# Kernel optimization log

Hardware: AMD Instinct MI355X
Metric: run time of the kernel (lower is better)

The kernel has to match this reference:

```python
import jax, jax.numpy as jnp
import numpy as np

D_STATE = 512
D_MODEL = 512
BATCH = 8
SEQ = 4096
DT_MIN, DT_MAX = 1e-3, 0.1
LN_EPS = 1e-5


def setup_inputs() -> dict:
    key = jax.random.key(0)
    ks = jax.random.split(key, 4)
    x = jax.random.normal(ks[0], (BATCH, SEQ, D_MODEL), dtype=jnp.float32)
    volatility_scale = jax.random.uniform(ks[1], (BATCH, SEQ, 1), dtype=jnp.float32)
    # parameters (mirroring the torch module's __init__)
    log_lambda_real = jnp.linspace(np.log(DT_MIN), np.log(DT_MAX), D_STATE).astype(jnp.float32)
    log_b = jax.random.uniform(ks[2], (D_STATE, 1), dtype=jnp.float32, minval=-0.5, maxval=0.5)
    c = jax.random.normal(ks[3], (1, D_STATE), dtype=jnp.float32) / np.sqrt(D_STATE)
    log_d = jnp.zeros((1,), jnp.float32)
    ts = np.array([1.0 / 24.0, 1.0, 5.0, 21.0, 63.0], np.float32)
    extra = np.linspace(63.0, 189.0, D_STATE - len(ts), dtype=np.float32)
    log_step = jnp.log(jnp.asarray(np.concatenate([ts, extra])))
    volatility_gate = jnp.ones((D_MODEL,), jnp.float32)
    alpha = jnp.asarray(0.7, jnp.float32)
    ln_weight = jnp.ones((D_STATE,), jnp.float32)
    ln_bias = jnp.zeros((D_STATE,), jnp.float32)
    return dict(x=x, volatility_scale=volatility_scale,
                log_lambda_real=log_lambda_real, log_b=log_b, c=c, log_d=log_d,
                log_step=log_step, volatility_gate=volatility_gate, alpha=alpha,
                ln_weight=ln_weight, ln_bias=ln_bias)


def reference(x, volatility_scale, log_lambda_real, log_b, c, log_d,
              log_step, volatility_gate, alpha, ln_weight, ln_bias):
    lam = -jnp.exp(log_lambda_real)              # [N], negative real poles
    step = jnp.exp(log_step)                     # [N], per-state timescale
    b = jnp.exp(log_b)[:, 0]                     # [N]
    d = jnp.exp(log_d)                           # [1], skip gain
    # bilinear (Tustin) discretization, paired per state
    z = step * lam                               # [N]
    a_disc = (2.0 + z) / (2.0 - z)               # [N]
    b_disc = step * (1.0 + a_disc) * b / 2.0     # [N]
    gate = jax.nn.sigmoid(volatility_gate)       # [D]
    c_vec = c[0]                                 # [N]

    def layer_norm(h):
        mu = jnp.mean(h, axis=-1, keepdims=True)
        var = jnp.var(h, axis=-1, keepdims=True)
        return (h - mu) * jax.lax.rsqrt(var + LN_EPS) * ln_weight + ln_bias

    def scan_step(h, inp):
        x_t, v_t = inp                           # [B,D], [B,1]
        h = a_disc * h + b_disc * x_t            # diagonal SSM update, [B,N]
        h = layer_norm(h)
        h = h / (1.0 + gate * v_t)               # volatility gating
        y_t = jnp.sum(h * c_vec, axis=-1, keepdims=True) + d * x_t  # [B,D]
        return h, y_t

    h0 = jnp.zeros((x.shape[0], a_disc.shape[0]), x.dtype)
    xs = (jnp.swapaxes(x, 0, 1), jnp.swapaxes(volatility_scale, 0, 1))  # time-major
    _, ys = jax.lax.scan(scan_step, h0, xs)      # [S,B,D]
    y = jnp.swapaxes(ys, 0, 1)                   # [B,S,D]
    al = jax.nn.sigmoid(alpha)
    return al * x + (1.0 - al) * y
```

## Files before the change

kernel.cpp:

```cpp
#include <hip/hip_runtime.h>
#include <cstdint>
#include <cstddef>

#define BATCH 8
#define SEQ   4096
#define DS    512
#define JPL   8
#define BLK   8
#define NBLK  (SEQ / BLK)

typedef float v2f __attribute__((ext_vector_type(2)));
typedef float v4f __attribute__((ext_vector_type(4)));

static __device__ __forceinline__ v2f lo2(v4f x) { return __builtin_shufflevector(x, x, 0, 1); }
static __device__ __forceinline__ v2f hi2(v4f x) { return __builtin_shufflevector(x, x, 2, 3); }

template <int CTRL>
__device__ __forceinline__ float dpp_add(float v) {
  int t = __builtin_amdgcn_update_dpp(0, __builtin_bit_cast(int, v), CTRL, 0xF, 0xF, true);
  return v + __builtin_bit_cast(float, t);
}
__device__ __forceinline__ float wave_sum64(float v) {
  v = dpp_add<0x111>(v);
  v = dpp_add<0x112>(v);
  v = dpp_add<0x114>(v);
  v = dpp_add<0x118>(v);
  v = dpp_add<0x142>(v);
  v = dpp_add<0x143>(v);
  return v;
}
__device__ __forceinline__ float bcast63(float v) {
  return __builtin_bit_cast(float, __builtin_amdgcn_readlane(__builtin_bit_cast(int, v), 63));
}

__device__ __forceinline__ void ld16(const float* g, float* l) {
  __builtin_amdgcn_global_load_lds(
      (const __attribute__((address_space(1))) void*)g,
      (__attribute__((address_space(3))) void*)l, 16, 0, 0);
}

__global__ __launch_bounds__(192, 1) void ssm_scan(
    const float* __restrict__ x, const float* __restrict__ vol,
    const float* __restrict__ llr, const float* __restrict__ logb,
    const float* __restrict__ cvec, const float* __restrict__ lstp,
    const float* __restrict__ vgat, const float* __restrict__ lnw,
    const float* __restrict__ lnb, float* __restrict__ sp)
{
  __shared__ float X0[4096], X1[4096];
  __shared__ float R0[4096], R1[4096];
  __shared__ float SC0[512], SC1[512];

  const int b    = blockIdx.x;
  const int lane = threadIdx.x & 63;
  const int wid  = threadIdx.x >> 6;

  if (wid == 1) {
    const float* xg = x + (size_t)b * SEQ * DS + lane * JPL;
    float* spb = sp + (size_t)b * SEQ;

    auto dma_blk = [&](int blk, float* Xs) {
#pragma unroll
      for (int u = 0; u < BLK; ++u) {
        const float* row = xg + (size_t)(blk * BLK + u) * DS;
        ld16(row,     Xs + u * 512);
        ld16(row + 4, Xs + u * 512 + 256);
      }
    };
    auto red_copy = [&](const float* SCs, int blk) {
      float s[BLK];
#pragma unroll
      for (int u = 0; u < BLK; ++u) s[u] = wave_sum64(SCs[u * 64 + lane]);
      if (lane == 63) {
#pragma unroll
        for (int u = 0; u < BLK; ++u) spb[blk * BLK + u] = s[u];
      }
    };

    dma_blk(0, X0);
    __syncthreads();
#pragma unroll 1
    for (int i2 = 0; i2 < NBLK; i2 += 2) {
      dma_blk(i2 + 1, X1);
      if (i2 > 0) red_copy(SC1, i2 - 1);
      __syncthreads();
      if (i2 + 2 < NBLK) dma_blk(i2 + 2, X0);
      red_copy(SC0, i2);
      __syncthreads();
    }
    red_copy(SC1, NBLK - 1);
  } else if (wid == 2) {
    v2f gate[4];
#pragma unroll
    for (int j = 0; j < JPL; ++j)
      gate[j >> 1][j & 1] = 1.0f / (1.0f + expf(-vgat[lane * JPL + j]));
    const float* vg = vol + (size_t)b * SEQ;

    auto rg_blk = [&](v4f Va, v4f Vb, float* Rs) {
#pragma unroll
      for (int u = 0; u < BLK; ++u) {
        float vt = (u < 4) ? Va[u] : Vb[u - 4];
        v4f r0, r1;
#pragma unroll
        for (int k = 0; k < 4; ++k) {
          v2f den = gate[k] * vt + 1.0f;
          float q0 = __builtin_amdgcn_rcpf(den.x);
          float q1 = __builtin_amdgcn_rcpf(den.y);
          if (k < 2) { r0[2 * k] = q0; r0[2 * k + 1] = q1; }
          else       { r1[2 * (k - 2)] = q0; r1[2 * (k - 2) + 1] = q1; }
        }
        *(v4f*)(Rs + u * 512 + lane * 4)       = r0;
        *(v4f*)(Rs + u * 512 + 256 + lane * 4) = r1;
      }
    };

    v4f V0a = *(const v4f*)(vg + 0), V0b = *(const v4f*)(vg + 4);
    v4f V1a = *(const v4f*)(vg + 8), V1b = *(const v4f*)(vg + 12);
    rg_blk(V0a, V0b, R0);
    __syncthreads();
#pragma unroll 1
    for (int i2 = 0; i2 < NBLK; i2 += 2) {
      if (i2 + 2 < NBLK) {
        V0a = *(const v4f*)(vg + (i2 + 2) * BLK);
        V0b = *(const v4f*)(vg + (i2 + 2) * BLK + 4);
      }
      rg_blk(V1a, V1b, R1);
      __syncthreads();
      if (i2 + 3 < NBLK) {
        V1a = *(const v4f*)(vg + (i2 + 3) * BLK);
        V1b = *(const v4f*)(vg + (i2 + 3) * BLK + 4);
      }
      if (i2 + 2 < NBLK) rg_blk(V0a, V0b, R0);
      __syncthreads();
    }
  } else {
    v2f a[4], bd[4], w[4], bias[4], cc[4];
#pragma unroll
    for (int j = 0; j < JPL; ++j) {
      int n = lane * JPL + j;
      float lam = -expf(llr[n]);
      float st  = expf(lstp[n]);
      float z   = st * lam;
      float ad  = (2.0f + z) / (2.0f - z);
      a[j >> 1][j & 1]    = ad;
      bd[j >> 1][j & 1]   = st * (1.0f + ad) * expf(logb[n]) * 0.5f;
      w[j >> 1][j & 1]    = lnw[n];
      bias[j >> 1][j & 1] = lnb[n];
      cc[j >> 1][j & 1]   = cvec[n];
    }
    v2f h[4];
#pragma unroll
    for (int k = 0; k < 4; ++k) h[k] = (v2f){0.0f, 0.0f};

    auto proc_blk = [&](const float* Xs, const float* Rs, float* SCs) {
#pragma unroll
      for (int u = 0; u < BLK; ++u) {
        v4f xx0 = *(const v4f*)(Xs + u * 512 + lane * 4);
        v4f xx1 = *(const v4f*)(Xs + u * 512 + 256 + lane * 4);
        v4f rr0 = *(const v4f*)(Rs + u * 512 + lane * 4);
        v4f rr1 = *(const v4f*)(Rs + u * 512 + 256 + lane * 4);
        v2f xs[4] = {lo2(xx0), hi2(xx0), lo2(xx1), hi2(xx1)};
        v2f rs[4] = {lo2(rr0), hi2(rr0), lo2(rr1), hi2(rr1)};

        v2f hr[4];
#pragma unroll
        for (int k = 0; k < 4; ++k)
          hr[k] = __builtin_elementwise_fma(a[k], h[k], bd[k] * xs[k]);

        v2f ts = (hr[0] + hr[1]) + (hr[2] + hr[3]);
        float s1 = ts.x + ts.y;
        v2f qs = (hr[0] * hr[0] + hr[1] * hr[1]) + (hr[2] * hr[2] + hr[3] * hr[3]);
        float s2 = qs.x + qs.y;

        s1 = bcast63(wave_sum64(s1));
        s2 = bcast63(wave_sum64(s2));
        float mu  = s1 * (1.0f / DS);
        float m2  = s2 * (1.0f / DS);
        float var = __builtin_fmaf(-mu, mu, m2);
        float inv = __builtin_amdgcn_rsqf(var + 1e-5f);

#pragma unroll
        for (int k = 0; k < 4; ++k) {
          v2f niw = w[k] * inv;
          v2f hb  = bias[k] - niw * mu;
          v2f hln = __builtin_elementwise_fma(hr[k], niw, hb);
          h[k] = hln * rs[k];
        }

        v2f d = h[0] * cc[0];
        d = __builtin_elementwise_fma(h[1], cc[1], d);
        d = __builtin_elementwise_fma(h[2], cc[2], d);
        d = __builtin_elementwise_fma(h[3], cc[3], d);
        SCs[u * 64 + lane] = d.x + d.y;
      }
    };

    __syncthreads();
#pragma unroll 1
    for (int i2 = 0; i2 < NBLK; i2 += 2) {
      proc_blk(X0, R0, SC0);
      __syncthreads();
      proc_blk(X1, R1, SC1);
      __syncthreads();
    }
  }
}

__global__ __launch_bounds__(256) void out_scalar(
    const float* __restrict__ x, const float* __restrict__ sp,
    const float* __restrict__ alpha_p, const float* __restrict__ logd_p,
    float* __restrict__ out)
{
  const int lane = threadIdx.x & 63;
  const size_t bt = (size_t)blockIdx.x * 4 + (threadIdx.x >> 6);

  float al   = 1.0f / (1.0f + expf(-alpha_p[0]));
  float dd   = expf(logd_p[0]);
  float coef = __builtin_fmaf(1.0f - al, dd, al);
  float c1   = 1.0f - al;

  float s = sp[bt] * c1;
  const v4f* x4 = (const v4f*)x;
  v4f* o4 = (v4f*)out;
  size_t base = bt * 128;
#pragma unroll
  for (int j = 0; j < 2; ++j) {
    size_t i = base + lane + (size_t)j * 64;
    v4f xv = x4[i];
    o4[i] = xv * coef + s;
  }
}

extern "C" void kernel_launch(void* const* d_in, const int* in_sizes, int n_in,
                              void* d_out, int out_size, void* d_ws, size_t ws_size,
                              hipStream_t stream) {
  const float* x    = (const float*)d_in[0];
  const float* vol  = (const float*)d_in[1];
  const float* llr  = (const float*)d_in[2];
  const float* logb = (const float*)d_in[3];
  const float* cvec = (const float*)d_in[4];
  const float* logd = (const float*)d_in[5];
  const float* lstp = (const float*)d_in[6];
  const float* vgat = (const float*)d_in[7];
  const float* alph = (const float*)d_in[8];
  const float* lnw  = (const float*)d_in[9];
  const float* lnb  = (const float*)d_in[10];
  float* sp   = (float*)d_ws;
  float* outf = (float*)d_out;

  ssm_scan<<<BATCH, 192, 0, stream>>>(x, vol, llr, logb, cvec, lstp,
                                      vgat, lnw, lnb, sp);
  out_scalar<<<BATCH * SEQ / 4, 256, 0, stream>>>(x, sp, alph, logd, outf);
}
```

Baseline: 697.2 us.

## Double block size, prefetch next timestep LDS loads, interleave paired wave reductions

Raises the per-block timestep count from 8 to 16, which halves the number of barrier synchronisations between the producer waves and the compute wave. The compute wave now loads the next timestep's x and gating values from LDS while working on the current one, hiding LDS latency on the serial critical path. The two DPP wave reductions for mean and mean-square are interleaved so their dependency chains can overlap. LDS use doubles to about 132KB and register pressure rises, which could limit scheduling.

Measured after the change: 800.5 us. +14.8%, slower.

```diff
diff --git a/kernel.cpp b/kernel.cpp
--- a/kernel.cpp
+++ b/kernel.cpp
@@ -6,7 +6,7 @@
 #define SEQ   4096
 #define DS    512
 #define JPL   8
-#define BLK   8
+#define BLK   16
 #define NBLK  (SEQ / BLK)
 
 typedef float v2f __attribute__((ext_vector_type(2)));
@@ -29,6 +29,14 @@
   v = dpp_add<0x143>(v);
   return v;
 }
+__device__ __forceinline__ void wave_sum64x2(float& p, float& q) {
+  p = dpp_add<0x111>(p); q = dpp_add<0x111>(q);
+  p = dpp_add<0x112>(p); q = dpp_add<0x112>(q);
+  p = dpp_add<0x114>(p); q = dpp_add<0x114>(q);
+  p = dpp_add<0x118>(p); q = dpp_add<0x118>(q);
+  p = dpp_add<0x142>(p); q = dpp_add<0x142>(q);
+  p = dpp_add<0x143>(p); q = dpp_add<0x143>(q);
+}
 __device__ __forceinline__ float bcast63(float v) {
   return __builtin_bit_cast(float, __builtin_amdgcn_readlane(__builtin_bit_cast(int, v), 63));
 }
@@ -46,9 +54,9 @@
     const float* __restrict__ vgat, const float* __restrict__ lnw,
     const float* __restrict__ lnb, float* __restrict__ sp)
 {
-  __shared__ float X0[4096], X1[4096];
-  __shared__ float R0[4096], R1[4096];
-  __shared__ float SC0[512], SC1[512];
+  __shared__ float X0[BLK * 512], X1[BLK * 512];
+  __shared__ float R0[BLK * 512], R1[BLK * 512];
+  __shared__ float SC0[BLK * 64], SC1[BLK * 64];
 
   const int b    = blockIdx.x;
   const int lane = threadIdx.x & 63;
@@ -95,10 +103,10 @@
       gate[j >> 1][j & 1] = 1.0f / (1.0f + expf(-vgat[lane * JPL + j]));
     const float* vg = vol + (size_t)b * SEQ;
 
-    auto rg_blk = [&](v4f Va, v4f Vb, float* Rs) {
+    auto rg_blk = [&](const v4f (&V)[4], float* Rs) {
 #pragma unroll
       for (int u = 0; u < BLK; ++u) {
-        float vt = (u < 4) ? Va[u] : Vb[u - 4];
+        float vt = V[u >> 2][u & 3];
         v4f r0, r1;
 #pragma unroll
         for (int k = 0; k < 4; ++k) {
@@ -112,24 +120,23 @@
         *(v4f*)(Rs + u * 512 + 256 + lane * 4) = r1;
       }
     };
-
-    v4f V0a = *(const v4f*)(vg + 0), V0b = *(const v4f*)(vg + 4);
-    v4f V1a = *(const v4f*)(vg + 8), V1b = *(const v4f*)(vg + 12);
-    rg_blk(V0a, V0b, R0);
+    auto vload = [&](v4f (&V)[4], int blk) {
+#pragma unroll
+      for (int k = 0; k < 4; ++k) V[k] = *(const v4f*)(vg + blk * BLK + k * 4);
+    };
+
+    v4f V0[4], V1[4];
+    vload(V0, 0);
+    vload(V1, 1);
+    rg_blk(V0, R0);
     __syncthreads();
 #pragma unroll 1
     for (int i2 = 0; i2 < NBLK; i2 += 2) {
-      if (i2 + 2 < NBLK) {
-        V0a = *(const v4f*)(vg + (i2 + 2) * BLK);
-        V0b = *(const v4f*)(vg + (i2 + 2) * BLK + 4);
-      }
-      rg_blk(V1a, V1b, R1);
-      __syncthreads();
-      if (i2 + 3 < NBLK) {
-        V1a = *(const v4f*)(vg + (i2 + 3) * BLK);
-        V1b = *(const v4f*)(vg + (i2 + 3) * BLK + 4);
-      }
-      if (i2 + 2 < NBLK) rg_blk(V0a, V0b, R0);
+      if (i2 + 2 < NBLK) vload(V0, i2 + 2);
+      rg_blk(V1, R1);
+      __syncthreads();
+      if (i2 + 3 < NBLK) vload(V1, i2 + 3);
+      if (i2 + 2 < NBLK) rg_blk(V0, R0);
       __syncthreads();
     }
   } else {
@@ -152,14 +159,22 @@
     for (int k = 0; k < 4; ++k) h[k] = (v2f){0.0f, 0.0f};
 
     auto proc_blk = [&](const float* Xs, const float* Rs, float* SCs) {
+      const float* xq = Xs + lane * 4;
+      const float* rq = Rs + lane * 4;
+      v4f xx0 = *(const v4f*)(xq);
+      v4f xx1 = *(const v4f*)(xq + 256);
+      v4f rr0 = *(const v4f*)(rq);
+      v4f rr1 = *(const v4f*)(rq + 256);
 #pragma unroll
       for (int u = 0; u < BLK; ++u) {
-        v4f xx0 = *(const v4f*)(Xs + u * 512 + lane * 4);
-        v4f xx1 = *(const v4f*)(Xs + u * 512 + 256 + lane * 4);
-        v4f rr0 = *(const v4f*)(Rs + u * 512 + lane * 4);
-        v4f rr1 = *(const v4f*)(Rs + u * 512 + 256 + lane * 4);
         v2f xs[4] = {lo2(xx0), hi2(xx0), lo2(xx1), hi2(xx1)};
         v2f rs[4] = {lo2(rr0), hi2(rr0), lo2(rr1), hi2(rr1)};
+        if (u + 1 < BLK) {
+          xx0 = *(const v4f*)(xq + (u + 1) * 512);
+          xx1 = *(const v4f*)(xq + (u + 1) * 512 + 256);
+          rr0 = *(const v4f*)(rq + (u + 1) * 512);
+          rr1 = *(const v4f*)(rq + (u + 1) * 512 + 256);
+        }
 
         v2f hr[4];
 #pragma unroll
@@ -171,8 +186,9 @@
         v2f qs = (hr[0] * hr[0] + hr[1] * hr[1]) + (hr[2] * hr[2] + hr[3] * hr[3]);
         float s2 = qs.x + qs.y;
 
-        s1 = bcast63(wave_sum64(s1));
-        s2 = bcast63(wave_sum64(s2));
+        wave_sum64x2(s1, s2);
+        s1 = bcast63(s1);
+        s2 = bcast63(s2);
         float mu  = s1 * (1.0f / DS);
         float m2  = s2 * (1.0f / DS);
         float var = __builtin_fmaf(-mu, mu, m2);
```
